# Performance work log

Hardware: AMD Instinct MI355X
Metric: run time of the kernel (lower is better)

## Reference

```python
import jax, jax.numpy as jnp
import numpy as np

N_NODES = 100000
N_EDGES = 6400000
N_ORDERS = 4
EPO = N_EDGES // N_ORDERS  # edges per order
K = 10


def setup_inputs() -> dict:
    key = jax.random.key(0)
    ks = jax.random.split(key, 7)
    x = jax.random.normal(ks[0], (N_NODES, K), dtype=jnp.float32)
    w_mp = jax.random.normal(ks[1], (K, 2 * K), dtype=jnp.float32) * (1.0 / np.sqrt(2 * K))
    b_mp = jax.random.normal(ks[2], (K,), dtype=jnp.float32) * 0.01
    w_out = jax.random.normal(ks[3], (K, K), dtype=jnp.float32) * (1.0 / np.sqrt(K))
    b_out = jax.random.normal(ks[4], (K,), dtype=jnp.float32) * 0.01
    edge_index = jax.random.randint(ks[5], (2, N_EDGES), 0, N_NODES, dtype=jnp.int64)
    orders = jax.random.randint(ks[6], (N_ORDERS, EPO), 0, N_EDGES, dtype=jnp.int64)
    return {"x": x, "w_mp": w_mp, "b_mp": b_mp, "w_out": w_out,
            "b_out": b_out, "edge_index": edge_index, "orders": orders}


def reference(x, w_mp, b_mp, w_out, b_out, edge_index, orders):
    n = x.shape[0]

    def step(h, order_idx):
        ei = edge_index[:, order_idx]            # [2, EPO] edges of this order
        # torch code swaps rows [1,0] before propagate, so in PyG terms:
        # source j = original row 1, target i = original row 0
        dst = ei[0]
        src = ei[1]
        x_i = h[dst]                             # [EPO, K]
        x_j = h[src]                             # [EPO, K]
        msg_in = jnp.concatenate([x_i, x_j - x_i], axis=1)   # [EPO, 2K]
        msg = msg_in @ w_mp.T + b_mp             # [EPO, K]
        aggr = jax.ops.segment_sum(msg, dst, num_segments=n)  # scatter-add
        return aggr + h, None                    # update(): aggr_out + x

    h, _ = jax.lax.scan(step, x, orders)
    return h @ w_out.T + b_out
```

## Files before the change

### kernel.cpp

```cpp
#include <hip/hip_runtime.h>

#define BLK 256
#define WBITS 14
#define W1CAP 17408
#define CAPBP 7168
#define MAXNW 512
#define MAXK2 2048
#define MAXNBD 512
#define OVFN 65536
#define IPTA 32
#define NSL2 17
#define SENT 0xFFFFFFFFu

__global__ void k_init_h(const float* __restrict__ x, float* __restrict__ h, int n) {
    int total = n * 16;
    int gs = gridDim.x * blockDim.x;
    for (int i = blockIdx.x * blockDim.x + threadIdx.x; i < total; i += gs) {
        int row = i >> 4, col = i & 15;
        h[i] = (col < 10) ? x[row * 10 + col] : 0.0f;
    }
}

__global__ __launch_bounds__(512) void k_win(const int* __restrict__ orders,
                                             int total, int epo, int NW,
                                             int* __restrict__ gcnt1,
                                             unsigned* __restrict__ recs1,
                                             int* __restrict__ ovf1_cnt,
                                             unsigned* __restrict__ ovf1) {
    __shared__ int bcnt[MAXNW];
    __shared__ int gbase[MAXNW];
    int t = threadIdx.x;
    for (int i = t; i < NW; i += 512) bcnt[i] = 0;
    __syncthreads();

    size_t base = (size_t)blockIdx.x * (512 * IPTA);
    int st0 = (int)(base / (size_t)epo);
    size_t b1 = (size_t)(st0 + 1) * (size_t)epo;

    unsigned recr[IPTA]; int rr[IPTA];
    #pragma unroll
    for (int q = 0; q < IPTA; ++q) {
        size_t g = base + (size_t)q * 512 + t;
        recr[q] = SENT; rr[q] = 0;
        if (g < (size_t)total) {
            int idx = orders[g];
            int st = (g >= b1) ? (st0 + 1) : st0;
            recr[q] = ((unsigned)st << 23) | (unsigned)idx;
            rr[q] = atomicAdd(&bcnt[idx >> WBITS], 1);
        }
    }
    __syncthreads();
    for (int k = t; k < NW; k += 512) {
        int c = bcnt[k];
        gbase[k] = c ? atomicAdd(&gcnt1[k], c) : 0;
    }
    __syncthreads();
    #pragma unroll
    for (int q = 0; q < IPTA; ++q) {
        if (recr[q] != SENT) {
            int idx = (int)(recr[q] & 0x7FFFFFu);
            int key = idx >> WBITS;
            int pos = gbase[key] + rr[q];
            if (pos < W1CAP)
                recs1[(size_t)key * W1CAP + pos] = recr[q];
            else {
                int o = atomicAdd(ovf1_cnt, 1);
                if (o < OVFN) ovf1[o] = recr[q];
            }
        }
    }
}

__global__ __launch_bounds__(1024) void k_bin2(const int* __restrict__ ei, int ne,
                                               const int* __restrict__ gcnt1,
                                               const unsigned* __restrict__ recs1,
                                               int NW, int NBD,
                                               int* __restrict__ gcnt2,
                                               unsigned* __restrict__ recs2,
                                               int* __restrict__ ovf2_cnt,
                                               int2* __restrict__ ovf2) {
    __shared__ int cnt2[MAXK2];
    __shared__ int gbase[MAXK2];
    int t = threadIdx.x;
    int K2 = 4 * NBD;
    for (int i = t; i < K2; i += 1024) cnt2[i] = 0;
    __syncthreads();

    int w = blockIdx.x;
    int c = gcnt1[w]; if (c > W1CAP) c = W1CAP;
    const unsigned* strm = recs1 + (size_t)w * W1CAP;

    int recr[NSL2];
    #pragma unroll
    for (int q = 0; q < NSL2; ++q) {
        int r = q * 1024 + t;
        recr[q] = (r < c) ? (int)strm[r] : -1;
    }
    int dv[NSL2];
    #pragma unroll
    for (int q = 0; q < NSL2; ++q)
        dv[q] = (recr[q] >= 0) ? ei[recr[q] & 0x7FFFFF] : 0;
    unsigned meta[NSL2];
    #pragma unroll
    for (int q = 0; q < NSL2; ++q) {
        meta[q] = SENT;
        if (recr[q] >= 0) {
            int st = (int)(((unsigned)recr[q]) >> 23);
            int key = st * NBD + (dv[q] >> 8);
            int rk = atomicAdd(&cnt2[key], 1);
            meta[q] = ((unsigned)dv[q] << 15) | (unsigned)rk;
        }
    }
    __syncthreads();
    for (int k = t; k < K2; k += 1024) {
        int cc = cnt2[k];
        gbase[k] = cc ? atomicAdd(&gcnt2[k], (cc + 15) & ~15) : 0;
    }
    __syncthreads();
    #pragma unroll
    for (int q = 0; q < NSL2; ++q) {
        if (meta[q] != SENT) {
            int idx = recr[q] & 0x7FFFFF;
            int st  = (int)(((unsigned)recr[q]) >> 23);
            int s = ei[(size_t)ne + idx];
            int d = (int)(meta[q] >> 15);
            int rk = (int)(meta[q] & 0x7FFFu);
            int key = st * NBD + (d >> 8);
            int pos = gbase[key] + rk;
            unsigned r2 = ((unsigned)(d & 255) << 20) | (unsigned)s;
            if (pos < CAPBP)
                recs2[(size_t)key * CAPBP + pos] = r2;
            else {
                int o = atomicAdd(ovf2_cnt, 1);
                if (o < OVFN) ovf2[o] = make_int2((st << 18) | d, s);
            }
        }
    }
    for (int k = t; k < K2; k += 1024) {
        int cc = cnt2[k];
        if (cc) {
            int b0 = gbase[k];
            int pe = b0 + ((cc + 15) & ~15);
            if (pe > CAPBP) pe = CAPBP;
            unsigned* sp = recs2 + (size_t)k * CAPBP;
            for (int p = b0 + cc; p < pe; ++p) sp[p] = SENT;
        }
    }
}

#define IPTG ((CAPBP + 511) / 512)
template<bool FINAL>
__global__ __launch_bounds__(512) void k_agg2(const float* __restrict__ h_cur,
                                              float* __restrict__ h_next,
                                              const int* __restrict__ gcnt2_st,
                                              const unsigned* __restrict__ recs2_st,
                                              const float* __restrict__ w_mp,
                                              const float* __restrict__ b_mp,
                                              const float* __restrict__ w_out,
                                              const float* __restrict__ b_out,
                                              float* __restrict__ out, int n) {
    __shared__ unsigned srt[CAPBP];
    __shared__ int cnts[256];
    __shared__ int sc[256];
    __shared__ int offs[257];
    __shared__ float part[256 * 10];
    __shared__ float Wa[100], Wb[100], Bm[10];
    __shared__ float Wo[100], Bo[10];
    int t = threadIdx.x;
    if (t < 100) {
        int k = t / 10, j = t - k * 10;
        float w1 = w_mp[k * 20 + j];
        float w2 = w_mp[k * 20 + 10 + j];
        Wa[t] = w1 - w2; Wb[t] = w2;
        if (FINAL) Wo[t] = w_out[t];
    }
    if (t < 10) { Bm[t] = b_mp[t]; if (FINAL) Bo[t] = b_out[t]; }
    if (t < 256) cnts[t] = 0;
    __syncthreads();

    int bkt = blockIdx.x;
    int cnt = gcnt2_st[bkt];
    if (cnt > CAPBP) cnt = CAPBP;
    const unsigned* strm = recs2_st + (size_t)bkt * CAPBP;

    unsigned myrec[IPTG];
    #pragma unroll
    for (int q = 0; q < IPTG; ++q) {
        int r = q * 512 + t;
        myrec[q] = SENT;
        if (r < cnt) {
            unsigned rec = strm[r];
            if (rec != SENT) {
                myrec[q] = rec;
                atomicAdd(&cnts[rec >> 20], 1);
            }
        }
    }
    __syncthreads();

    if (t < 256) sc[t] = cnts[t];
    __syncthreads();
    for (int off = 1; off < 256; off <<= 1) {
        int v = (t < 256 && t >= off) ? sc[t - off] : 0;
        __syncthreads();
        if (t < 256) sc[t] += v;
        __syncthreads();
    }
    if (t < 256) offs[t + 1] = sc[t];
    if (t == 0) offs[0] = 0;
    __syncthreads();
    if (t < 256) cnts[t] = offs[t];
    __syncthreads();

    #pragma unroll
    for (int q = 0; q < IPTG; ++q) {
        if (myrec[q] != SENT) {
            int pos = atomicAdd(&cnts[myrec[q] >> 20], 1);
            srt[pos] = myrec[q];
        }
    }
    __syncthreads();

    int node = t & 255, half = t >> 8;
    int b0 = offs[node], m = offs[node + 1] - b0;
    float S[10] = {0,0,0,0,0,0,0,0,0,0};
    for (int p = b0 + half; p < b0 + m; p += 2) {
        int s = (int)(srt[p] & 0xFFFFFu);
        const float* pj = h_cur + (size_t)s * 16;
        float4 a0 = *(const float4*)(pj);
        float4 a1 = *(const float4*)(pj + 4);
        float2 a2 = *(const float2*)(pj + 8);
        S[0] += a0.x; S[1] += a0.y; S[2] += a0.z; S[3] += a0.w;
        S[4] += a1.x; S[5] += a1.y; S[6] += a1.z; S[7] += a1.w;
        S[8] += a2.x; S[9] += a2.y;
    }
    if (half == 1) {
        #pragma unroll
        for (int j = 0; j < 10; ++j) part[node * 10 + j] = S[j];
    }
    __syncthreads();
    if (half == 0) {
        int i = bkt * 256 + node;
        if (i < n) {
            #pragma unroll
            for (int j = 0; j < 10; ++j) S[j] += part[node * 10 + j];
            const float* pi = h_cur + (size_t)i * 16;
            float4 x0 = *(const float4*)(pi);
            float4 x1 = *(const float4*)(pi + 4);
            float2 x2 = *(const float2*)(pi + 8);
            float xi[10] = {x0.x, x0.y, x0.z, x0.w, x1.x, x1.y, x1.z, x1.w, x2.x, x2.y};
            float deg = (float)m;
            float o[10];
            #pragma unroll
            for (int k = 0; k < 10; ++k) {
                float ma = Bm[k];
                float mb = 0.0f;
                #pragma unroll
                for (int j = 0; j < 10; ++j) {
                    ma += Wa[k * 10 + j] * xi[j];
                    mb += Wb[k * 10 + j] * S[j];
                }
                o[k] = xi[k] + deg * ma + mb;
            }
            if (FINAL) {
                float q2[10];
                #pragma unroll
                for (int k = 0; k < 10; ++k) {
                    float m2 = Bo[k];
                    #pragma unroll
                    for (int j = 0; j < 10; ++j) m2 += Wo[k * 10 + j] * o[j];
                    q2[k] = m2;
                }
                float* po = out + (size_t)i * 10;
                *(float2*)(po)     = make_float2(q2[0], q2[1]);
                *(float2*)(po + 2) = make_float2(q2[2], q2[3]);
                *(float2*)(po + 4) = make_float2(q2[4], q2[5]);
                *(float2*)(po + 6) = make_float2(q2[6], q2[7]);
                *(float2*)(po + 8) = make_float2(q2[8], q2[9]);
            } else {
                float* po = h_next + (size_t)i * 16;
                *(float4*)(po)     = make_float4(o[0], o[1], o[2], o[3]);
                *(float4*)(po + 4) = make_float4(o[4], o[5], o[6], o[7]);
                *(float2*)(po + 8) = make_float2(o[8], o[9]);
            }
        }
    }
}

__global__ void k_fix(const float* __restrict__ h_cur, float* __restrict__ h_next,
                      const int* __restrict__ ei, int ne,
                      const int* __restrict__ ovf1_cnt, const unsigned* __restrict__ ovf1,
                      const int* __restrict__ ovf2_cnt, const int2* __restrict__ ovf2,
                      const float* __restrict__ w_mp, const float* __restrict__ b_mp,
                      int st) {
    __shared__ float Wa[100], Wb[100], Bm[10];
    int t = threadIdx.x;
    if (t < 100) {
        int k = t / 10, j = t - k * 10;
        float w1 = w_mp[k * 20 + j];
        float w2 = w_mp[k * 20 + 10 + j];
        Wa[t] = w1 - w2; Wb[t] = w2;
    }
    if (t < 10) Bm[t] = b_mp[t];
    __syncthreads();
    int c1 = *ovf1_cnt; if (c1 > OVFN) c1 = OVFN;
    int c2 = *ovf2_cnt; if (c2 > OVFN) c2 = OVFN;
    int gs = gridDim.x * blockDim.x;
    for (int i = blockIdx.x * blockDim.x + t; i < c1 + c2; i += gs) {
        int d, s;
        if (i < c1) {
            unsigned v = ovf1[i];
            if ((int)(v >> 23) != st) continue;
            int idx = (int)(v & 0x7FFFFFu);
            d = ei[idx]; s = ei[(size_t)ne + idx];
        } else {
            int2 p = ovf2[i - c1];
            if ((p.x >> 18) != st) continue;
            d = p.x & 0x3FFFF; s = p.y;
        }
        const float* pi = h_cur + (size_t)d * 16;
        const float* pj = h_cur + (size_t)s * 16;
        float xi[10], xj[10];
        #pragma unroll
        for (int j = 0; j < 10; ++j) { xi[j] = pi[j]; xj[j] = pj[j]; }
        float* po = h_next + (size_t)d * 16;
        #pragma unroll
        for (int k = 0; k < 10; ++k) {
            float m = Bm[k];
            #pragma unroll
            for (int j = 0; j < 10; ++j) m += Wa[k * 10 + j] * xi[j] + Wb[k * 10 + j] * xj[j];
            atomicAdd(po + k, m);
        }
    }
}

__global__ void k_fix_final(const float* __restrict__ h_cur, float* __restrict__ out,
                            const int* __restrict__ ei, int ne,
                            const int* __restrict__ ovf1_cnt, const unsigned* __restrict__ ovf1,
                            const int* __restrict__ ovf2_cnt, const int2* __restrict__ ovf2,
                            const float* __restrict__ w_mp, const float* __restrict__ b_mp,
                            const float* __restrict__ w_out, int st) {
    __shared__ float Wa[100], Wb[100], Bm[10], Wo[100];
    int t = threadIdx.x;
    if (t < 100) {
        int k = t / 10, j = t - k * 10;
        float w1 = w_mp[k * 20 + j];
        float w2 = w_mp[k * 20 + 10 + j];
        Wa[t] = w1 - w2; Wb[t] = w2;
        Wo[t] = w_out[t];
    }
    if (t < 10) Bm[t] = b_mp[t];
    __syncthreads();
    int c1 = *ovf1_cnt; if (c1 > OVFN) c1 = OVFN;
    int c2 = *ovf2_cnt; if (c2 > OVFN) c2 = OVFN;
    int gs = gridDim.x * blockDim.x;
    for (int i = blockIdx.x * blockDim.x + t; i < c1 + c2; i += gs) {
        int d, s;
        if (i < c1) {
            unsigned v = ovf1[i];
            if ((int)(v >> 23) != st) continue;
            int idx = (int)(v & 0x7FFFFFu);
            d = ei[idx]; s = ei[(size_t)ne + idx];
        } else {
            int2 p = ovf2[i - c1];
            if ((p.x >> 18) != st) continue;
            d = p.x & 0x3FFFF; s = p.y;
        }
        const float* pi = h_cur + (size_t)d * 16;
        const float* pj = h_cur + (size_t)s * 16;
        float xi[10], xj[10];
        #pragma unroll
        for (int j = 0; j < 10; ++j) { xi[j] = pi[j]; xj[j] = pj[j]; }
        float dm[10];
        #pragma unroll
        for (int k = 0; k < 10; ++k) {
            float m = Bm[k];
            #pragma unroll
            for (int j = 0; j < 10; ++j) m += Wa[k * 10 + j] * xi[j] + Wb[k * 10 + j] * xj[j];
            dm[k] = m;
        }
        float* po = out + (size_t)d * 10;
        #pragma unroll
        for (int q = 0; q < 10; ++q) {
            float m = 0.0f;
            #pragma unroll
            for (int k = 0; k < 10; ++k) m += Wo[q * 10 + k] * dm[k];
            atomicAdd(po + q, m);
        }
    }
}


__global__ void k_init10(const float* __restrict__ x, float* __restrict__ h, int n10) {
    int gs = gridDim.x * blockDim.x;
    for (int i = blockIdx.x * blockDim.x + threadIdx.x; i < n10; i += gs) h[i] = x[i];
}
__global__ void k_copy4(const float4* __restrict__ src, float4* __restrict__ dst, int n4) {
    int gs = gridDim.x * blockDim.x;
    for (int i = blockIdx.x * blockDim.x + threadIdx.x; i < n4; i += gs) dst[i] = src[i];
}
__global__ void k_edge_step10(const float* __restrict__ h_cur, float* __restrict__ h_next,
                              const int* __restrict__ edge_index, const int* __restrict__ order,
                              const float* __restrict__ w_mp, const float* __restrict__ b_mp,
                              int epo, int ne) {
    __shared__ float Wc[200]; __shared__ float Bc[10];
    int t = threadIdx.x;
    if (t < 200) {
        int k = t / 20, j = t - k * 20;
        float w = w_mp[t];
        Wc[t] = (j < 10) ? (w - w_mp[k * 20 + j + 10]) : w;
    }
    if (t < 10) Bc[t] = b_mp[t];
    __syncthreads();
    int gs = gridDim.x * blockDim.x;
    for (int e = blockIdx.x * blockDim.x + t; e < epo; e += gs) {
        int idx = order[e];
        int dst = edge_index[idx];
        int src = edge_index[(size_t)ne + idx];
        const float* pi = h_cur + (size_t)dst * 10;
        const float* pj = h_cur + (size_t)src * 10;
        float xi[10], xj[10];
        #pragma unroll
        for (int j = 0; j < 10; ++j) { xi[j] = pi[j]; xj[j] = pj[j]; }
        float* po = h_next + (size_t)dst * 10;
        #pragma unroll
        for (int k = 0; k < 10; ++k) {
            float m = Bc[k];
            #pragma unroll
            for (int j = 0; j < 10; ++j) m += Wc[k * 20 + j] * xi[j] + Wc[k * 20 + 10 + j] * xj[j];
            atomicAdd(po + k, m);
        }
    }
}
__global__ void k_out10(const float* __restrict__ h, const float* __restrict__ w_out,
                        const float* __restrict__ b_out, float* __restrict__ out, int n) {
    __shared__ float W[100]; __shared__ float B[10];
    int t = threadIdx.x;
    if (t < 100) W[t] = w_out[t];
    if (t < 10)  B[t] = b_out[t];
    __syncthreads();
    int gs = gridDim.x * blockDim.x;
    for (int i = blockIdx.x * blockDim.x + t; i < n; i += gs) {
        float xi[10];
        #pragma unroll
        for (int j = 0; j < 10; ++j) xi[j] = h[(size_t)i * 10 + j];
        #pragma unroll
        for (int k = 0; k < 10; ++k) {
            float m = B[k];
            #pragma unroll
            for (int j = 0; j < 10; ++j) m += W[k * 10 + j] * xi[j];
            out[(size_t)i * 10 + k] = m;
        }
    }
}


extern "C" void kernel_launch(void* const* d_in, const int* in_sizes, int n_in,
                              void* d_out, int out_size, void* d_ws, size_t ws_size,
                              hipStream_t stream) {
    const float* x      = (const float*)d_in[0];
    const float* w_mp   = (const float*)d_in[1];
    const float* b_mp   = (const float*)d_in[2];
    const float* w_out  = (const float*)d_in[3];
    const float* b_out  = (const float*)d_in[4];
    const int*   edge_i = (const int*)d_in[5];
    const int*   orders = (const int*)d_in[6];

    int n  = in_sizes[0] / 10;
    int ne = in_sizes[5] / 2;
    const int n_orders = 4;
    int epo = in_sizes[6] / n_orders;
    int total = n_orders * epo;

    float* out = (float*)d_out;

    int NBD = (n + 255) >> 8;
    int NW  = (ne + (1 << WBITS) - 1) >> WBITS;
    int K2  = 4 * NBD;

    size_t off_hA    = 0;
    size_t off_hB    = off_hA + (size_t)n * 16;
    size_t off_recs1 = off_hB + (size_t)n * 16;
    size_t off_recs2 = off_recs1 + (size_t)NW * W1CAP;
    size_t off_ovf2  = off_recs2 + (size_t)K2 * CAPBP;
    size_t off_ovf1  = off_ovf2 + (size_t)2 * OVFN;
    size_t off_gcnt1 = off_ovf1 + OVFN;
    size_t off_gcnt2 = off_gcnt1 + NW;
    size_t off_cnts  = off_gcnt2 + K2;
    size_t need      = (off_cnts + 2) * 4;

    bool ok = (ws_size >= need) && (NW <= MAXNW) && (NBD <= MAXNBD) &&
              (K2 <= MAXK2) && (ne <= (1 << 23)) && (n < (1 << 17));

    if (!ok) {
        float* hA = (float*)d_ws;
        float* hB = hA + (size_t)n * 10;
        int n10 = n * 10;
        hipLaunchKernelGGL(k_init10, dim3(min((n10 + BLK - 1) / BLK, 2048)), dim3(BLK), 0, stream,
                           x, hA, n10);
        int n4 = n10 / 4;
        float* cur = hA; float* nxt = hB;
        int gb_edge = min((epo + BLK - 1) / BLK, 6400);
        for (int s = 0; s < n_orders; ++s) {
            hipLaunchKernelGGL(k_copy4, dim3(min((n4 + BLK - 1) / BLK, 2048)), dim3(BLK), 0, stream,
                               (const float4*)cur, (float4*)nxt, n4);
            hipLaunchKernelGGL(k_edge_step10, dim3(gb_edge), dim3(BLK), 0, stream,
                               cur, nxt, edge_i, orders + (size_t)s * epo, w_mp, b_mp, epo, ne);
            float* t2 = cur; cur = nxt; nxt = t2;
        }
        hipLaunchKernelGGL(k_out10, dim3(min((n + BLK - 1) / BLK, 2048)), dim3(BLK), 0, stream,
                           cur, w_out, b_out, out, n);
        return;
    }

    float*    hA      = (float*)d_ws;
    float*    hB      = (float*)d_ws + off_hB;
    unsigned* recs1   = (unsigned*)d_ws + off_recs1;
    unsigned* recs2   = (unsigned*)d_ws + off_recs2;
    int2*     ovf2    = (int2*)((int*)d_ws + off_ovf2);
    unsigned* ovf1    = (unsigned*)d_ws + off_ovf1;
    int*      gcnt1   = (int*)d_ws + off_gcnt1;
    int*      gcnt2   = (int*)d_ws + off_gcnt2;
    int*      ovfcnts = (int*)d_ws + off_cnts;

    hipMemsetAsync(gcnt1, 0, ((size_t)NW + (size_t)K2 + 2) * sizeof(int), stream);

    int gb_init = min((n * 16 + BLK - 1) / BLK, 2048);
    hipLaunchKernelGGL(k_init_h, dim3(gb_init), dim3(BLK), 0, stream, x, hA, n);

    int gbA = (total + 512 * IPTA - 1) / (512 * IPTA);
    hipLaunchKernelGGL(k_win, dim3(gbA), dim3(512), 0, stream,
                       orders, total, epo, NW, gcnt1, recs1, ovfcnts + 0, ovf1);

    hipLaunchKernelGGL(k_bin2, dim3(NW), dim3(1024), 0, stream,
                       edge_i, ne, gcnt1, recs1, NW, NBD,
                       gcnt2, recs2, ovfcnts + 1, ovf2);

    float* cur = hA; float* nxt = hB;
    for (int s = 0; s < n_orders; ++s) {
        bool fin = (s == n_orders - 1);
        if (fin) {
            hipLaunchKernelGGL((k_agg2<true>), dim3(NBD), dim3(512), 0, stream,
                               cur, nxt, gcnt2 + (size_t)s * NBD,
                               recs2 + (size_t)s * NBD * CAPBP, w_mp, b_mp,
                               w_out, b_out, out, n);
            hipLaunchKernelGGL(k_fix_final, dim3(8), dim3(256), 0, stream,
                               cur, out, edge_i, ne,
                               ovfcnts + 0, ovf1, ovfcnts + 1, ovf2,
                               w_mp, b_mp, w_out, s);
        } else {
            hipLaunchKernelGGL((k_agg2<false>), dim3(NBD), dim3(512), 0, stream,
                               cur, nxt, gcnt2 + (size_t)s * NBD,
                               recs2 + (size_t)s * NBD * CAPBP, w_mp, b_mp,
                               w_out, b_out, out, n);
            hipLaunchKernelGGL(k_fix, dim3(8), dim3(256), 0, stream,
                               cur, nxt, edge_i, ne,
                               ovfcnts + 0, ovf1, ovfcnts + 1, ovf2,
                               w_mp, b_mp, s);
            float* t2 = cur; cur = nxt; nxt = t2;
        }
    }
}
```

Measured before the change: 317.4 us.

## Replace global atomic binning with per-window local sort and gather in aggregation

The second binning pass now sorts each window's records in shared memory by (order, destination bucket) and writes them contiguously with per-window offset tables, instead of reserving space in global buckets via atomics and padding with sentinels. The aggregation kernel then gathers each bucket's segments from all windows into shared staging before the per-node sort. Window size is halved (more, smaller windows) to fit the shared-memory sort. This removes global atomics and padded, sparse bucket storage, but adds a serial per-thread gather over up to NW segments, with variable lengths, in the aggregation kernel, which runs for every order.

```diff
diff --git a/kernel.cpp b/kernel.cpp
--- a/kernel.cpp
+++ b/kernel.cpp
@@ -1,15 +1,15 @@
 #include <hip/hip_runtime.h>
 
 #define BLK 256
-#define WBITS 14
-#define W1CAP 17408
-#define CAPBP 7168
-#define MAXNW 512
+#define WBITS 13
+#define W1CAP 9216
+#define STCAP 4608
+#define MAXNW 1024
 #define MAXK2 2048
 #define MAXNBD 512
 #define OVFN 65536
 #define IPTA 32
-#define NSL2 17
+#define NSL 18
 #define SENT 0xFFFFFFFFu
 
 __global__ void k_init_h(const float* __restrict__ x, float* __restrict__ h, int n) {
@@ -71,98 +71,113 @@
     }
 }
 
-__global__ __launch_bounds__(1024) void k_bin2(const int* __restrict__ ei, int ne,
+__global__ __launch_bounds__(512) void k_bsort(const int* __restrict__ ei, int ne,
                                                const int* __restrict__ gcnt1,
                                                const unsigned* __restrict__ recs1,
-                                               int NW, int NBD,
-                                               int* __restrict__ gcnt2,
+                                               int NW, int NBD, int K2,
                                                unsigned* __restrict__ recs2,
-                                               int* __restrict__ ovf2_cnt,
-                                               int2* __restrict__ ovf2) {
+                                               int* __restrict__ blk_offs) {
+    __shared__ unsigned srt[W1CAP];
     __shared__ int cnt2[MAXK2];
-    __shared__ int gbase[MAXK2];
-    int t = threadIdx.x;
-    int K2 = 4 * NBD;
-    for (int i = t; i < K2; i += 1024) cnt2[i] = 0;
+    __shared__ int lofs[MAXK2 + 1];
+    __shared__ int sc[512];
+    int t = threadIdx.x;
+    for (int i = t; i < K2; i += 512) cnt2[i] = 0;
     __syncthreads();
 
     int w = blockIdx.x;
     int c = gcnt1[w]; if (c > W1CAP) c = W1CAP;
     const unsigned* strm = recs1 + (size_t)w * W1CAP;
 
-    int recr[NSL2];
+    int recr[NSL];
     #pragma unroll
-    for (int q = 0; q < NSL2; ++q) {
-        int r = q * 1024 + t;
+    for (int q = 0; q < NSL; ++q) {
+        int r = q * 512 + t;
         recr[q] = (r < c) ? (int)strm[r] : -1;
     }
-    int dv[NSL2];
+    int dv[NSL];
     #pragma unroll
-    for (int q = 0; q < NSL2; ++q)
+    for (int q = 0; q < NSL; ++q)
         dv[q] = (recr[q] >= 0) ? ei[recr[q] & 0x7FFFFF] : 0;
-    unsigned meta[NSL2];
+    unsigned meta[NSL];
     #pragma unroll
-    for (int q = 0; q < NSL2; ++q) {
+    for (int q = 0; q < NSL; ++q) {
         meta[q] = SENT;
         if (recr[q] >= 0) {
             int st = (int)(((unsigned)recr[q]) >> 23);
             int key = st * NBD + (dv[q] >> 8);
             int rk = atomicAdd(&cnt2[key], 1);
-            meta[q] = ((unsigned)dv[q] << 15) | (unsigned)rk;
-        }
-    }
-    __syncthreads();
-    for (int k = t; k < K2; k += 1024) {
-        int cc = cnt2[k];
-        gbase[k] = cc ? atomicAdd(&gcnt2[k], (cc + 15) & ~15) : 0;
-    }
-    __syncthreads();
+            meta[q] = ((unsigned)dv[q] << 14) | (unsigned)rk;
+        }
+    }
+    __syncthreads();
+
+    {
+        int v[4]; int sum = 0;
+        #pragma unroll
+        for (int i = 0; i < 4; ++i) {
+            int k = t * 4 + i;
+            v[i] = (k < K2) ? cnt2[k] : 0;
+            sum += v[i];
+        }
+        sc[t] = sum;
+        __syncthreads();
+        for (int off = 1; off < 512; off <<= 1) {
+            int u = (t >= off) ? sc[t - off] : 0;
+            __syncthreads();
+            sc[t] += u;
+            __syncthreads();
+        }
+        int run = sc[t] - sum;
+        #pragma unroll
+        for (int i = 0; i < 4; ++i) {
+            int k = t * 4 + i;
+            if (k <= K2) lofs[k] = run;
+            run += v[i];
+        }
+        if (t == 511) lofs[K2] = sc[511];
+    }
+    __syncthreads();
+
     #pragma unroll
-    for (int q = 0; q < NSL2; ++q) {
+    for (int q = 0; q < NSL; ++q) {
         if (meta[q] != SENT) {
             int idx = recr[q] & 0x7FFFFF;
             int st  = (int)(((unsigned)recr[q]) >> 23);
             int s = ei[(size_t)ne + idx];
-            int d = (int)(meta[q] >> 15);
-            int rk = (int)(meta[q] & 0x7FFFu);
+            int d = (int)(meta[q] >> 14);
+            int rk = (int)(meta[q] & 0x3FFFu);
             int key = st * NBD + (d >> 8);
-            int pos = gbase[key] + rk;
-            unsigned r2 = ((unsigned)(d & 255) << 20) | (unsigned)s;
-            if (pos < CAPBP)
-                recs2[(size_t)key * CAPBP + pos] = r2;
-            else {
-                int o = atomicAdd(ovf2_cnt, 1);
-                if (o < OVFN) ovf2[o] = make_int2((st << 18) | d, s);
-            }
-        }
-    }
-    for (int k = t; k < K2; k += 1024) {
-        int cc = cnt2[k];
-        if (cc) {
-            int b0 = gbase[k];
-            int pe = b0 + ((cc + 15) & ~15);
-            if (pe > CAPBP) pe = CAPBP;
-            unsigned* sp = recs2 + (size_t)k * CAPBP;
-            for (int p = b0 + cc; p < pe; ++p) sp[p] = SENT;
-        }
-    }
-}
-
-#define IPTG ((CAPBP + 511) / 512)
+            srt[lofs[key] + rk] = ((unsigned)(d & 255) << 20) | (unsigned)s;
+        }
+    }
+    __syncthreads();
+
+    unsigned* dst = recs2 + (size_t)w * W1CAP;
+    for (int r = t; r < c; r += 512) dst[r] = srt[r];
+    int* bo = blk_offs + (size_t)w * (K2 + 1);
+    for (int k = t; k <= K2; k += 512) bo[k] = lofs[k];
+}
+
 template<bool FINAL>
-__global__ __launch_bounds__(512) void k_agg2(const float* __restrict__ h_cur,
+__global__ __launch_bounds__(512) void k_agg3(const float* __restrict__ h_cur,
                                               float* __restrict__ h_next,
-                                              const int* __restrict__ gcnt2_st,
-                                              const unsigned* __restrict__ recs2_st,
+                                              const int* __restrict__ blk_offs,
+                                              const unsigned* __restrict__ recs2,
+                                              int NW, int K2, int NBD, int st,
                                               const float* __restrict__ w_mp,
                                               const float* __restrict__ b_mp,
                                               const float* __restrict__ w_out,
                                               const float* __restrict__ b_out,
-                                              float* __restrict__ out, int n) {
-    __shared__ unsigned srt[CAPBP];
+                                              float* __restrict__ out, int n,
+                                              int* __restrict__ ovf2_cnt,
+                                              int2* __restrict__ ovf2) {
+    __shared__ unsigned stage[STCAP];
+    __shared__ unsigned srt[STCAP];
     __shared__ int cnts[256];
     __shared__ int sc[256];
     __shared__ int offs[257];
+    __shared__ int cursor;
     __shared__ float part[256 * 10];
     __shared__ float Wa[100], Wb[100], Bm[10];
     __shared__ float Wo[100], Bo[10];
@@ -176,27 +191,36 @@
     }
     if (t < 10) { Bm[t] = b_mp[t]; if (FINAL) Bo[t] = b_out[t]; }
     if (t < 256) cnts[t] = 0;
+    if (t == 0) cursor = 0;
     __syncthreads();
 
     int bkt = blockIdx.x;
-    int cnt = gcnt2_st[bkt];
-    if (cnt > CAPBP) cnt = CAPBP;
-    const unsigned* strm = recs2_st + (size_t)bkt * CAPBP;
-
-    unsigned myrec[IPTG];
-    #pragma unroll
-    for (int q = 0; q < IPTG; ++q) {
-        int r = q * 512 + t;
-        myrec[q] = SENT;
-        if (r < cnt) {
-            unsigned rec = strm[r];
-            if (rec != SENT) {
-                myrec[q] = rec;
-                atomicAdd(&cnts[rec >> 20], 1);
+    int key = st * NBD + bkt;
+
+    for (int b = t; b < NW; b += 512) {
+        const int* bo = blk_offs + (size_t)b * (K2 + 1) + key;
+        int o0 = bo[0], o1 = bo[1];
+        int len = o1 - o0;
+        if (len > 0) {
+            int base = atomicAdd(&cursor, len);
+            const unsigned* src = recs2 + (size_t)b * W1CAP + o0;
+            for (int i = 0; i < len; ++i) {
+                unsigned rec = src[i];
+                int pos = base + i;
+                if (pos < STCAP) {
+                    stage[pos] = rec;
+                    atomicAdd(&cnts[rec >> 20], 1);
+                } else {
+                    int o = atomicAdd(ovf2_cnt, 1);
+                    if (o < OVFN)
+                        ovf2[o] = make_int2((st << 18) | (bkt * 256 + (int)(rec >> 20)),
+                                            (int)(rec & 0xFFFFFu));
+                }
             }
         }
     }
     __syncthreads();
+    int T = cursor; if (T > STCAP) T = STCAP;
 
     if (t < 256) sc[t] = cnts[t];
     __syncthreads();
@@ -212,12 +236,10 @@
     if (t < 256) cnts[t] = offs[t];
     __syncthreads();
 
-    #pragma unroll
-    for (int q = 0; q < IPTG; ++q) {
-        if (myrec[q] != SENT) {
-            int pos = atomicAdd(&cnts[myrec[q] >> 20], 1);
-            srt[pos] = myrec[q];
-        }
+    for (int r = t; r < T; r += 512) {
+        unsigned rec = stage[r];
+        int pos = atomicAdd(&cnts[rec >> 20], 1);
+        srt[pos] = rec;
     }
     __syncthreads();
 
@@ -482,11 +504,12 @@
     size_t off_hB    = off_hA + (size_t)n * 16;
     size_t off_recs1 = off_hB + (size_t)n * 16;
     size_t off_recs2 = off_recs1 + (size_t)NW * W1CAP;
-    size_t off_ovf2  = off_recs2 + (size_t)K2 * CAPBP;
+    size_t off_boffs = off_recs2 + (size_t)NW * W1CAP;
+    size_t off_ovf2  = off_boffs + (size_t)NW * (K2 + 1);
+    if (off_ovf2 & 1) off_ovf2++;
     size_t off_ovf1  = off_ovf2 + (size_t)2 * OVFN;
     size_t off_gcnt1 = off_ovf1 + OVFN;
-    size_t off_gcnt2 = off_gcnt1 + NW;
-    size_t off_cnts  = off_gcnt2 + K2;
+    size_t off_cnts  = off_gcnt1 + NW;
     size_t need      = (off_cnts + 2) * 4;
 
     bool ok = (ws_size >= need) && (NW <= MAXNW) && (NBD <= MAXNBD) &&
@@ -517,13 +540,13 @@
     float*    hB      = (float*)d_ws + off_hB;
     unsigned* recs1   = (unsigned*)d_ws + off_recs1;
     unsigned* recs2   = (unsigned*)d_ws + off_recs2;
+    int*      boffs   = (int*)d_ws + off_boffs;
     int2*     ovf2    = (int2*)((int*)d_ws + off_ovf2);
     unsigned* ovf1    = (unsigned*)d_ws + off_ovf1;
     int*      gcnt1   = (int*)d_ws + off_gcnt1;
-    int*      gcnt2   = (int*)d_ws + off_gcnt2;
     int*      ovfcnts = (int*)d_ws + off_cnts;
 
-    hipMemsetAsync(gcnt1, 0, ((size_t)NW + (size_t)K2 + 2) * sizeof(int), stream);
+    hipMemsetAsync(gcnt1, 0, ((size_t)NW + 2) * sizeof(int), stream);
 
     int gb_init = min((n * 16 + BLK - 1) / BLK, 2048);
     hipLaunchKernelGGL(k_init_h, dim3(gb_init), dim3(BLK), 0, stream, x, hA, n);
@@ -532,27 +555,26 @@
     hipLaunchKernelGGL(k_win, dim3(gbA), dim3(512), 0, stream,
                        orders, total, epo, NW, gcnt1, recs1, ovfcnts + 0, ovf1);
 
-    hipLaunchKernelGGL(k_bin2, dim3(NW), dim3(1024), 0, stream,
-                       edge_i, ne, gcnt1, recs1, NW, NBD,
-                       gcnt2, recs2, ovfcnts + 1, ovf2);
+    hipLaunchKernelGGL(k_bsort, dim3(NW), dim3(512), 0, stream,
+                       edge_i, ne, gcnt1, recs1, NW, NBD, K2, recs2, boffs);
 
     float* cur = hA; float* nxt = hB;
     for (int s = 0; s < n_orders; ++s) {
         bool fin = (s == n_orders - 1);
         if (fin) {
-            hipLaunchKernelGGL((k_agg2<true>), dim3(NBD), dim3(512), 0, stream,
-                               cur, nxt, gcnt2 + (size_t)s * NBD,
-                               recs2 + (size_t)s * NBD * CAPBP, w_mp, b_mp,
-                               w_out, b_out, out, n);
+            hipLaunchKernelGGL((k_agg3<true>), dim3(NBD), dim3(512), 0, stream,
+                               cur, nxt, boffs, recs2, NW, K2, NBD, s,
+                               w_mp, b_mp, w_out, b_out, out, n,
+                               ovfcnts + 1, ovf2);
             hipLaunchKernelGGL(k_fix_final, dim3(8), dim3(256), 0, stream,
                                cur, out, edge_i, ne,
                                ovfcnts + 0, ovf1, ovfcnts + 1, ovf2,
                                w_mp, b_mp, w_out, s);
         } else {
-            hipLaunchKernelGGL((k_agg2<false>), dim3(NBD), dim3(512), 0, stream,
-                               cur, nxt, gcnt2 + (size_t)s * NBD,
-                               recs2 + (size_t)s * NBD * CAPBP, w_mp, b_mp,
-                               w_out, b_out, out, n);
+            hipLaunchKernelGGL((k_agg3<false>), dim3(NBD), dim3(512), 0, stream,
+                               cur, nxt, boffs, recs2, NW, K2, NBD, s,
+                               w_mp, b_mp, w_out, b_out, out, n,
+                               ovfcnts + 1, ovf2);
             hipLaunchKernelGGL(k_fix, dim3(8), dim3(256), 0, stream,
                                cur, nxt, edge_i, ne,
                                ovfcnts + 0, ovf1, ovfcnts + 1, ovf2,
```

Result: faster. 287.0 us, median of 2 (-9.6%).
